# Performance work log

Measured on AMD Instinct MI355X. Metric: run time of the kernel, lower is better.

## Reference

```python
import jax, jax.numpy as jnp
import numpy as np

_pi = np.pi
CONST_FACTOR = np.array([
    1/np.sqrt(4*_pi),
    2*_pi/3*np.sqrt(3/(4*_pi)), 2*_pi/3*np.sqrt(3/(4*_pi)), 2*_pi/3*np.sqrt(3/(4*_pi)),
    _pi/4*3*np.sqrt(5/(12*_pi)), _pi/4*3*np.sqrt(5/(12*_pi)), _pi/4*3*np.sqrt(5/(12*_pi)),
    _pi/4*(3/2)*np.sqrt(5/(12*_pi)), _pi/4*(1/2)*np.sqrt(5/(4*_pi))], dtype=np.float32)


def setup_inputs() -> dict:
    key = jax.random.key(0)
    ks = jax.random.split(key, 8)
    B, V, F, H, W, U = 4, 5023, 9976, 512, 512, 256
    vertices = jax.random.normal(ks[0], (B, V, 3), jnp.float32)
    transformed_vertices = jax.random.normal(ks[1], (B, V, 3), jnp.float32)
    albedos = jax.random.uniform(ks[2], (B, 3, U, U), jnp.float32)
    lights = jax.random.normal(ks[3], (B, 9, 3), jnp.float32) * 0.3
    faces = jax.random.randint(ks[4], (F, 3), 0, V, jnp.int32)
    face_uvcoords = jax.random.uniform(ks[5], (1, F, 3, 3), jnp.float32, minval=-1.0, maxval=1.0)
    # rasterizer outputs (external CUDA kernel): -1 == no face hit
    pix_to_face = jax.random.randint(ks[6], (B, H, W, 1), 0, F + 1, jnp.int32) - 1
    b = jax.random.uniform(ks[7], (B, H, W, 1, 3), jnp.float32) + 1e-3
    bary_coords = b / b.sum(-1, keepdims=True)
    return dict(vertices=vertices, transformed_vertices=transformed_vertices,
                albedos=albedos, lights=lights, face_uvcoords=face_uvcoords,
                bary_coords=bary_coords, faces=faces, pix_to_face=pix_to_face)


def _vertex_normals(vertices, faces):
    vf = vertices[:, faces]                    # [B,F,3,3] face-vertex gather
    v0, v1, v2 = vf[:, :, 0], vf[:, :, 1], vf[:, :, 2]
    B, V = vertices.shape[:2]
    n = jnp.zeros((B, V, 3), vertices.dtype)
    n = n.at[:, faces[:, 1]].add(jnp.cross(v2 - v1, v0 - v1))
    n = n.at[:, faces[:, 2]].add(jnp.cross(v0 - v2, v1 - v2))
    n = n.at[:, faces[:, 0]].add(jnp.cross(v1 - v0, v2 - v0))
    return n / jnp.clip(jnp.linalg.norm(n, axis=-1, keepdims=True), 1e-6)


def _grid_sample(img, grid):
    # torch F.grid_sample bilinear, align_corners=False, zero padding
    # img [B,C,Hi,Wi], grid [B,Ho,Wo,2] (x,y) in [-1,1]
    B, C, Hi, Wi = img.shape
    x = (grid[..., 0] + 1.0) * (Wi * 0.5) - 0.5
    y = (grid[..., 1] + 1.0) * (Hi * 0.5) - 0.5
    x0 = jnp.floor(x); y0 = jnp.floor(y)
    wx = x - x0; wy = y - y0

    def fetch(xi, yi):
        xi_i = xi.astype(jnp.int32); yi_i = yi.astype(jnp.int32)
        valid = ((xi_i >= 0) & (xi_i < Wi) & (yi_i >= 0) & (yi_i < Hi)).astype(img.dtype)
        xc = jnp.clip(xi_i, 0, Wi - 1); yc = jnp.clip(yi_i, 0, Hi - 1)
        vals = jax.vmap(lambda im, yy, xx: im[:, yy, xx])(img, yc, xc)  # [B,C,Ho,Wo]
        return vals * valid[:, None]

    return (fetch(x0, y0) * ((1 - wx) * (1 - wy))[:, None]
            + fetch(x0 + 1, y0) * (wx * (1 - wy))[:, None]
            + fetch(x0, y0 + 1) * ((1 - wx) * wy)[:, None]
            + fetch(x0 + 1, y0 + 1) * (wx * wy)[:, None])


def reference(vertices, transformed_vertices, albedos, lights, face_uvcoords,
              bary_coords, faces, pix_to_face):
    sg = jax.lax.stop_gradient
    B = vertices.shape[0]
    cf = jnp.asarray(CONST_FACTOR)

    # depth normalization (global min/max as in torch)
    z = transformed_vertices[:, :, 2]
    z = z - z.min(); z = z / z.max(); z = z * 80.0 + 10.0
    tv = transformed_vertices.at[:, :, 2].set(z)

    face_vertice = vertices[:, faces]                        # [B,F,3,3]
    normals = _vertex_normals(vertices, faces)
    face_normals = normals[:, faces]                         # [B,F,3,3]
    t_normals = _vertex_normals(tv, faces)
    t_face_normals = t_normals[:, faces]                     # [B,F,3,3]

    attributes = jnp.concatenate([
        jnp.broadcast_to(face_uvcoords, (B,) + face_uvcoords.shape[1:]),
        sg(t_face_normals), sg(face_vertice), face_normals], -1)  # [B,F,3,12]

    # barycentric interpolation (Pytorch3dRasterizer.forward tail)
    mask = pix_to_face < 0                                   # [B,H,W,1]
    safe = jnp.where(mask, 0, pix_to_face)
    pfv = attributes[jnp.arange(B)[:, None, None, None], safe]   # [B,H,W,1,3,12]
    pv = (bary_coords[..., None] * pfv).sum(-2)              # [B,H,W,1,12]
    pv = jnp.where(mask[..., None], 0.0, pv)
    pv = pv[:, :, :, 0].transpose(0, 3, 1, 2)                # [B,12,H,W]
    vismask = (~mask[..., 0]).astype(pv.dtype)[:, None]      # [B,1,H,W]
    rendering = jnp.concatenate([pv, vismask], 1)            # [B,13,H,W]

    # albedo sampling via UV grid
    grid = rendering[:, :2].transpose(0, 2, 3, 1)            # [B,H,W,2]
    albedo_images = _grid_sample(albedos, grid)              # [B,3,H,W]

    # spherical harmonic shading (add_SHlight, lights [B,9,3])
    N = rendering[:, 9:12]                                   # [B,3,H,W]
    one = jnp.ones_like(N[:, 0])
    sh = jnp.stack([one, N[:, 0], N[:, 1], N[:, 2],
                    N[:, 0] * N[:, 1], N[:, 0] * N[:, 2], N[:, 1] * N[:, 2],
                    N[:, 0] ** 2 - N[:, 1] ** 2, 3.0 * N[:, 2] ** 2 - 1.0], 1)  # [B,9,H,W]
    sh = sh * cf[None, :, None, None]
    shading = (lights[:, :, :, None, None] * sh[:, :, None]).sum(1)  # [B,3,H,W]

    images = albedo_images * shading
    return images
```

## Files before the change

kernel.cpp:

```cpp
#include <hip/hip_runtime.h>
#include <hip/hip_fp16.h>
#include <math.h>

#define NB 4
#define NV 5023
#define NF 9976
#define NH 512
#define NW 512
#define NU 256

__device__ __constant__ float d_cf[9] = {
    0.28209479177387814f,
    1.0233267079464885f,
    1.0233267079464885f,
    1.0233267079464885f,
    0.8580855308091875f,
    0.8580855308091875f,
    0.8580855308091875f,
    0.42904276540459376f,
    0.24770795610037571f
};

#define NRM_FLOATS  (NB * NV * 3)
#define ZERO_BLOCKS ((NRM_FLOATS + 255) / 256)
#define FACE_ITEMS  (NB * NF)
#define FACE_BLOCKS ((FACE_ITEMS + 255) / 256)

#define ACELLS 257
#define AINT2_ITEMS  (NB * ACELLS * ACELLS)
#define AINT2_BLOCKS ((AINT2_ITEMS + 255) / 256)

__device__ inline float pack2h(float a, float b) {
    __half2 h = __halves2half2(__float2half_rn(a), __float2half_rn(b));
    union { __half2 h; float f; } u; u.h = h; return u.f;
}
__device__ inline float2 unpack2h(float f) {
    union { float f; __half2 h; } u; u.f = f;
    return __half22float2(u.h);
}
__device__ inline float pack2s(float a, float b) {
    unsigned int lo = (unsigned short)(short)__float2int_rn(a * 32767.0f);
    unsigned int hi = (unsigned short)(short)__float2int_rn(b * 32767.0f);
    return __uint_as_float(lo | (hi << 16));
}
__device__ inline float2 unpack2s(float f) {
    unsigned int u = __float_as_uint(f);
    const float s = 1.0f / 32767.0f;
    return make_float2((float)(short)(u & 0xffffu) * s,
                       (float)(short)(u >> 16) * s);
}
__device__ inline unsigned int packu10(float r, float g, float b) {
    unsigned int qr = (unsigned int)__float2int_rn(r * 1023.0f);
    unsigned int qg = (unsigned int)__float2int_rn(g * 1023.0f);
    unsigned int qb = (unsigned int)__float2int_rn(b * 1023.0f);
    return qr | (qg << 10) | (qb << 20);
}

__global__ void init_kernel(float*       __restrict__ nrm,
                            const float* __restrict__ albedos,
                            const float* __restrict__ lights,
                            uint4*       __restrict__ aint2,
                            float*       __restrict__ lsbuf) {
    if (blockIdx.x < ZERO_BLOCKS) {
        int i = blockIdx.x * blockDim.x + threadIdx.x;
        if (i < NRM_FLOATS) nrm[i] = 0.0f;
        if (i < NB * 27) {
            int b = i / 27;
            int kc = i - b * 27;
            lsbuf[i] = lights[b * 27 + kc] * d_cf[kc / 3] * (1.0f / 1023.0f);
        }
    } else {
        int j = (blockIdx.x - ZERO_BLOCKS) * blockDim.x + threadIdx.x;
        if (j >= AINT2_ITEMS) return;
        int b = j / (ACELLS * ACELLS);
        int rc = j - b * (ACELLS * ACELLS);
        int r = rc / ACELLS;
        int c = rc - r * ACELLS;

        const float* ab = albedos + (size_t)b * 3 * NU * NU;
        uint4 cell = make_uint4(0u, 0u, 0u, 0u);

        int x0 = c - 1, x1 = c;
        int y0 = r - 1, y1 = r;
        bool vx0 = (x0 >= 0);
        bool vx1 = (x1 <= NU - 1);
        bool vy0 = (y0 >= 0);
        bool vy1 = (y1 <= NU - 1);

        if (vy0) {
            int row = y0 * NU;
            if (vx0) { int o = row + x0;
                cell.x = packu10(ab[o], ab[NU*NU + o], ab[2*NU*NU + o]); }
            if (vx1) { int o = row + x1;
                cell.y = packu10(ab[o], ab[NU*NU + o], ab[2*NU*NU + o]); }
        }
        if (vy1) {
            int row = y1 * NU;
            if (vx0) { int o = row + x0;
                cell.z = packu10(ab[o], ab[NU*NU + o], ab[2*NU*NU + o]); }
            if (vx1) { int o = row + x1;
                cell.w = packu10(ab[o], ab[NU*NU + o], ab[2*NU*NU + o]); }
        }
        aint2[j] = cell;
    }
}

__global__ void face_accum_kernel(const float* __restrict__ verts,
                                  const int*   __restrict__ faces,
                                  float*       __restrict__ nrm) {
    int idx = blockIdx.x * blockDim.x + threadIdx.x;
    if (idx >= FACE_ITEMS) return;
    int b = idx / NF;
    int f = idx - b * NF;

    int i0 = faces[f * 3 + 0];
    int i1 = faces[f * 3 + 1];
    int i2 = faces[f * 3 + 2];

    const float* vb = verts + (size_t)b * NV * 3;
    float v0x = vb[i0 * 3 + 0], v0y = vb[i0 * 3 + 1], v0z = vb[i0 * 3 + 2];
    float v1x = vb[i1 * 3 + 0], v1y = vb[i1 * 3 + 1], v1z = vb[i1 * 3 + 2];
    float v2x = vb[i2 * 3 + 0], v2y = vb[i2 * 3 + 1], v2z = vb[i2 * 3 + 2];

    float ax = v1x - v0x, ay = v1y - v0y, az = v1z - v0z;
    float bx = v2x - v0x, by = v2y - v0y, bz = v2z - v0z;
    float cx = ay * bz - az * by;
    float cy = az * bx - ax * bz;
    float cz = ax * by - ay * bx;

    float* nb = nrm + (size_t)b * NV * 3;
    atomicAdd(&nb[i0 * 3 + 0], cx);
    atomicAdd(&nb[i0 * 3 + 1], cy);
    atomicAdd(&nb[i0 * 3 + 2], cz);
    atomicAdd(&nb[i1 * 3 + 0], cx);
    atomicAdd(&nb[i1 * 3 + 1], cy);
    atomicAdd(&nb[i1 * 3 + 2], cz);
    atomicAdd(&nb[i2 * 3 + 0], cx);
    atomicAdd(&nb[i2 * 3 + 1], cy);
    atomicAdd(&nb[i2 * 3 + 2], cz);
}

__global__ void pack_kernel(const float* __restrict__ nrm,
                            const int*   __restrict__ faces,
                            const float* __restrict__ uvc,
                            float4*      __restrict__ recs) {
    int idx = blockIdx.x * blockDim.x + threadIdx.x;
    if (idx >= FACE_ITEMS) return;
    int b = idx / NF;
    int f = idx - b * NF;

    int i0 = faces[f * 3 + 0];
    int i1 = faces[f * 3 + 1];
    int i2 = faces[f * 3 + 2];

    const float* nb = nrm + (size_t)b * NV * 3;
    float n0x = nb[i0 * 3 + 0], n0y = nb[i0 * 3 + 1], n0z = nb[i0 * 3 + 2];
    float n1x = nb[i1 * 3 + 0], n1y = nb[i1 * 3 + 1], n1z = nb[i1 * 3 + 2];
    float n2x = nb[i2 * 3 + 0], n2y = nb[i2 * 3 + 1], n2z = nb[i2 * 3 + 2];

    float l0 = 1.0f / fmaxf(sqrtf(n0x*n0x + n0y*n0y + n0z*n0z), 1e-6f);
    float l1 = 1.0f / fmaxf(sqrtf(n1x*n1x + n1y*n1y + n1z*n1z), 1e-6f);
    float l2 = 1.0f / fmaxf(sqrtf(n2x*n2x + n2y*n2y + n2z*n2z), 1e-6f);

    const float* uvf = uvc + (size_t)f * 9;

    float4 q0, q1;
    q0.x = pack2s(uvf[0], uvf[1]);
    q0.y = pack2s(uvf[3], uvf[4]);
    q0.z = pack2s(uvf[6], uvf[7]);
    q0.w = pack2h(n0x * l0, n0y * l0);
    q1.x = pack2h(n0z * l0, n1x * l1);
    q1.y = pack2h(n1y * l1, n1z * l1);
    q1.z = pack2h(n2x * l2, n2y * l2);
    q1.w = pack2h(n2z * l2, 0.0f);

    recs[(size_t)idx * 2 + 0] = q0;
    recs[(size_t)idx * 2 + 1] = q1;
}

__global__ void render_kernel(const float4* __restrict__ recs,
                              const uint4* __restrict__ aint2,
                              const float* __restrict__ lsbuf,
                              const float4* __restrict__ bary4,
                              const int4*  __restrict__ p2f4,
                              float*       __restrict__ out) {
    const int blk = blockIdx.x;
    const int xcd = blk & 7;
    const int b   = xcd >> 1;
    const int j   = ((blk >> 3) << 1) | (xcd & 1);
    const int q   = j * 256 + threadIdx.x;
    const int p   = q * 4;

    const int pixq = (b * NH * NW) / 4 + q;
    const int4 f4 = p2f4[pixq];
    const float4 bq0 = bary4[pixq * 3 + 0];
    const float4 bq1 = bary4[pixq * 3 + 1];
    const float4 bq2 = bary4[pixq * 3 + 2];

    const float* Ls = lsbuf + b * 27;

    const int fs[4] = {f4.x, f4.y, f4.z, f4.w};
    const float bw[12] = {bq0.x, bq0.y, bq0.z,  bq0.w, bq1.x, bq1.y,
                          bq1.z, bq1.w, bq2.x,  bq2.y, bq2.z, bq2.w};

    const float4* rb = recs + (size_t)b * NF * 2;
    const uint4* ab = aint2 + (size_t)b * ACELLS * ACELLS;

    float outv[3][4];

    #pragma unroll
    for (int px = 0; px < 4; ++px) {
        const int f = fs[px];
        float b0 = bw[px * 3 + 0], b1 = bw[px * 3 + 1], b2 = bw[px * 3 + 2];

        float u = 0.f, v = 0.f, nx = 0.f, ny = 0.f, nz = 0.f;
        if (f >= 0) {
            float4 q0 = rb[(size_t)f * 2 + 0];
            float4 q1 = rb[(size_t)f * 2 + 1];
            float2 uv0 = unpack2s(q0.x);
            float2 uv1 = unpack2s(q0.y);
            float2 uv2 = unpack2s(q0.z);
            float2 hA  = unpack2h(q0.w);
            float2 hB  = unpack2h(q1.x);
            float2 hC  = unpack2h(q1.y);
            float2 hD  = unpack2h(q1.z);
            float2 hE  = unpack2h(q1.w);

            u  = b0 * uv0.x + b1 * uv1.x + b2 * uv2.x;
            v  = b0 * uv0.y + b1 * uv1.y + b2 * uv2.y;
            nx = b0 * hA.x + b1 * hB.y + b2 * hD.x;
            ny = b0 * hA.y + b1 * hC.x + b2 * hD.y;
            nz = b0 * hB.x + b1 * hC.y + b2 * hE.x;
        }

        float x = (u + 1.0f) * (NU * 0.5f) - 0.5f;
        float y = (v + 1.0f) * (NU * 0.5f) - 0.5f;
        float x0f = floorf(x);
        float y0f = floorf(y);
        float wx = x - x0f;
        float wy = y - y0f;
        int ci = (int)x0f + 1;
        int ri = (int)y0f + 1;

        uint4 cell = ab[ri * ACELLS + ci];

        float iwx = 1.0f - wx, iwy = 1.0f - wy;
        float w00 = iwx * iwy, w10 = wx * iwy, w01 = iwx * wy, w11 = wx * wy;

        float a0 = w00 * (float)(cell.x & 1023u)
                 + w10 * (float)(cell.y & 1023u)
                 + w01 * (float)(cell.z & 1023u)
                 + w11 * (float)(cell.w & 1023u);
        float a1 = w00 * (float)((cell.x >> 10) & 1023u)
                 + w10 * (float)((cell.y >> 10) & 1023u)
                 + w01 * (float)((cell.z >> 10) & 1023u)
                 + w11 * (float)((cell.w >> 10) & 1023u);
        float a2 = w00 * (float)((cell.x >> 20) & 1023u)
                 + w10 * (float)((cell.y >> 20) & 1023u)
                 + w01 * (float)((cell.z >> 20) & 1023u)
                 + w11 * (float)((cell.w >> 20) & 1023u);

        float sh[9];
        sh[0] = 1.0f;
        sh[1] = nx;
        sh[2] = ny;
        sh[3] = nz;
        sh[4] = nx * ny;
        sh[5] = nx * nz;
        sh[6] = ny * nz;
        sh[7] = nx * nx - ny * ny;
        sh[8] = 3.0f * nz * nz - 1.0f;

        float s0 = 0.f, s1 = 0.f, s2 = 0.f;
        #pragma unroll
        for (int k = 0; k < 9; ++k) {
            s0 += Ls[k * 3 + 0] * sh[k];
            s1 += Ls[k * 3 + 1] * sh[k];
            s2 += Ls[k * 3 + 2] * sh[k];
        }

        outv[0][px] = a0 * s0;
        outv[1][px] = a1 * s1;
        outv[2][px] = a2 * s2;
    }

    const size_t hw = (size_t)NH * NW;
    #pragma unroll
    for (int c = 0; c < 3; ++c) {
        float4* op = (float4*)(out + ((size_t)b * 3 + c) * hw + p);
        *op = make_float4(outv[c][0], outv[c][1], outv[c][2], outv[c][3]);
    }
}

extern "C" void kernel_launch(void* const* d_in, const int* in_sizes, int n_in,
                              void* d_out, int out_size, void* d_ws, size_t ws_size,
                              hipStream_t stream) {
    const float* vertices = (const float*)d_in[0];
    const float* albedos  = (const float*)d_in[2];
    const float* lights   = (const float*)d_in[3];
    const float* uvc      = (const float*)d_in[4];
    const float* bary     = (const float*)d_in[5];
    const int*   faces    = (const int*)d_in[6];
    const int*   p2f      = (const int*)d_in[7];
    float*       out      = (float*)d_out;

    char* ws = (char*)d_ws;
    float* nrm = (float*)ws;
    size_t nrm_bytes = (size_t)NB * NV * 3 * sizeof(float);
    size_t off = (nrm_bytes + 255) & ~(size_t)255;
    float4* recs = (float4*)(ws + off);
    off += (size_t)FACE_ITEMS * 32;
    off = (off + 255) & ~(size_t)255;
    uint4* aint2 = (uint4*)(ws + off);
    off += (size_t)AINT2_ITEMS * sizeof(uint4);
    off = (off + 255) & ~(size_t)255;
    float* lsbuf = (float*)(ws + off);

    {
        init_kernel<<<ZERO_BLOCKS + AINT2_BLOCKS, 256, 0, stream>>>(
            nrm, albedos, lights, aint2, lsbuf);
    }
    {
        face_accum_kernel<<<FACE_BLOCKS, 256, 0, stream>>>(vertices, faces, nrm);
    }
    {
        pack_kernel<<<FACE_BLOCKS, 256, 0, stream>>>(nrm, faces, uvc, recs);
    }
    {
        render_kernel<<<NB * 256, 256, 0, stream>>>(recs, aint2, lsbuf,
                                                    (const float4*)bary,
                                                    (const int4*)p2f, out);
    }
}
```

Baseline: 48.95 us.

## Fuse normal accumulation and face packing via grid-wide spin barrier

Merges the face normal scatter-add kernel and the per-face packing kernel into one kernel of 160 blocks, which together cover all faces. A global atomic counter, reset in the init kernel, serves as a grid barrier so that every atomic accumulation lands before normals are read back and packed. The goal is to save one kernel launch and the inter-kernel gap. The cost is that correctness now depends on all 160 blocks being resident at once, and on the spin barrier adding latency.

```diff
diff --git a/kernel.cpp b/kernel.cpp
--- a/kernel.cpp
+++ b/kernel.cpp
@@ -24,7 +24,7 @@
 #define NRM_FLOATS  (NB * NV * 3)
 #define ZERO_BLOCKS ((NRM_FLOATS + 255) / 256)
 #define FACE_ITEMS  (NB * NF)
-#define FACE_BLOCKS ((FACE_ITEMS + 255) / 256)
+#define AP_BLOCKS   160
 
 #define ACELLS 257
 #define AINT2_ITEMS  (NB * ACELLS * ACELLS)
@@ -56,11 +56,12 @@
     return qr | (qg << 10) | (qb << 20);
 }
 
-__global__ void init_kernel(float*       __restrict__ nrm,
-                            const float* __restrict__ albedos,
-                            const float* __restrict__ lights,
-                            uint4*       __restrict__ aint2,
-                            float*       __restrict__ lsbuf) {
+__global__ void init_kernel(float*        __restrict__ nrm,
+                            const float*  __restrict__ albedos,
+                            const float*  __restrict__ lights,
+                            uint4*        __restrict__ aint2,
+                            float*        __restrict__ lsbuf,
+                            unsigned int* __restrict__ bar) {
     if (blockIdx.x < ZERO_BLOCKS) {
         int i = blockIdx.x * blockDim.x + threadIdx.x;
         if (i < NRM_FLOATS) nrm[i] = 0.0f;
@@ -69,6 +70,7 @@
             int kc = i - b * 27;
             lsbuf[i] = lights[b * 27 + kc] * d_cf[kc / 3] * (1.0f / 1023.0f);
         }
+        if (blockIdx.x == 0 && threadIdx.x == 0) bar[0] = 0u;
     } else {
         int j = (blockIdx.x - ZERO_BLOCKS) * blockDim.x + threadIdx.x;
         if (j >= AINT2_ITEMS) return;
@@ -105,77 +107,82 @@
     }
 }
 
-__global__ void face_accum_kernel(const float* __restrict__ verts,
-                                  const int*   __restrict__ faces,
-                                  float*       __restrict__ nrm) {
-    int idx = blockIdx.x * blockDim.x + threadIdx.x;
-    if (idx >= FACE_ITEMS) return;
-    int b = idx / NF;
-    int f = idx - b * NF;
-
-    int i0 = faces[f * 3 + 0];
-    int i1 = faces[f * 3 + 1];
-    int i2 = faces[f * 3 + 2];
-
-    const float* vb = verts + (size_t)b * NV * 3;
-    float v0x = vb[i0 * 3 + 0], v0y = vb[i0 * 3 + 1], v0z = vb[i0 * 3 + 2];
-    float v1x = vb[i1 * 3 + 0], v1y = vb[i1 * 3 + 1], v1z = vb[i1 * 3 + 2];
-    float v2x = vb[i2 * 3 + 0], v2y = vb[i2 * 3 + 1], v2z = vb[i2 * 3 + 2];
-
-    float ax = v1x - v0x, ay = v1y - v0y, az = v1z - v0z;
-    float bx = v2x - v0x, by = v2y - v0y, bz = v2z - v0z;
-    float cx = ay * bz - az * by;
-    float cy = az * bx - ax * bz;
-    float cz = ax * by - ay * bx;
-
-    float* nb = nrm + (size_t)b * NV * 3;
-    atomicAdd(&nb[i0 * 3 + 0], cx);
-    atomicAdd(&nb[i0 * 3 + 1], cy);
-    atomicAdd(&nb[i0 * 3 + 2], cz);
-    atomicAdd(&nb[i1 * 3 + 0], cx);
-    atomicAdd(&nb[i1 * 3 + 1], cy);
-    atomicAdd(&nb[i1 * 3 + 2], cz);
-    atomicAdd(&nb[i2 * 3 + 0], cx);
-    atomicAdd(&nb[i2 * 3 + 1], cy);
-    atomicAdd(&nb[i2 * 3 + 2], cz);
-}
-
-__global__ void pack_kernel(const float* __restrict__ nrm,
-                            const int*   __restrict__ faces,
-                            const float* __restrict__ uvc,
-                            float4*      __restrict__ recs) {
-    int idx = blockIdx.x * blockDim.x + threadIdx.x;
-    if (idx >= FACE_ITEMS) return;
-    int b = idx / NF;
-    int f = idx - b * NF;
-
-    int i0 = faces[f * 3 + 0];
-    int i1 = faces[f * 3 + 1];
-    int i2 = faces[f * 3 + 2];
-
-    const float* nb = nrm + (size_t)b * NV * 3;
-    float n0x = nb[i0 * 3 + 0], n0y = nb[i0 * 3 + 1], n0z = nb[i0 * 3 + 2];
-    float n1x = nb[i1 * 3 + 0], n1y = nb[i1 * 3 + 1], n1z = nb[i1 * 3 + 2];
-    float n2x = nb[i2 * 3 + 0], n2y = nb[i2 * 3 + 1], n2z = nb[i2 * 3 + 2];
-
-    float l0 = 1.0f / fmaxf(sqrtf(n0x*n0x + n0y*n0y + n0z*n0z), 1e-6f);
-    float l1 = 1.0f / fmaxf(sqrtf(n1x*n1x + n1y*n1y + n1z*n1z), 1e-6f);
-    float l2 = 1.0f / fmaxf(sqrtf(n2x*n2x + n2y*n2y + n2z*n2z), 1e-6f);
-
-    const float* uvf = uvc + (size_t)f * 9;
-
-    float4 q0, q1;
-    q0.x = pack2s(uvf[0], uvf[1]);
-    q0.y = pack2s(uvf[3], uvf[4]);
-    q0.z = pack2s(uvf[6], uvf[7]);
-    q0.w = pack2h(n0x * l0, n0y * l0);
-    q1.x = pack2h(n0z * l0, n1x * l1);
-    q1.y = pack2h(n1y * l1, n1z * l1);
-    q1.z = pack2h(n2x * l2, n2y * l2);
-    q1.w = pack2h(n2z * l2, 0.0f);
-
-    recs[(size_t)idx * 2 + 0] = q0;
-    recs[(size_t)idx * 2 + 1] = q1;
+__global__ void __launch_bounds__(256)
+accum_pack_kernel(const float*  __restrict__ verts,
+                  const int*    __restrict__ faces,
+                  const float*  __restrict__ uvc,
+                  float*        __restrict__ nrm,
+                  float4*       __restrict__ recs,
+                  unsigned int* __restrict__ bar) {
+    const int idx = blockIdx.x * blockDim.x + threadIdx.x;
+    int b = 0, f = 0, i0 = 0, i1 = 0, i2 = 0;
+
+    if (idx < FACE_ITEMS) {
+        b = idx / NF;
+        f = idx - b * NF;
+        i0 = faces[f * 3 + 0];
+        i1 = faces[f * 3 + 1];
+        i2 = faces[f * 3 + 2];
+
+        const float* vb = verts + (size_t)b * NV * 3;
+        float v0x = vb[i0*3+0], v0y = vb[i0*3+1], v0z = vb[i0*3+2];
+        float v1x = vb[i1*3+0], v1y = vb[i1*3+1], v1z = vb[i1*3+2];
+        float v2x = vb[i2*3+0], v2y = vb[i2*3+1], v2z = vb[i2*3+2];
+
+        float ax = v1x - v0x, ay = v1y - v0y, az = v1z - v0z;
+        float bx = v2x - v0x, by = v2y - v0y, bz = v2z - v0z;
+        float cx = ay * bz - az * by;
+        float cy = az * bx - ax * bz;
+        float cz = ax * by - ay * bx;
+
+        float* nb = nrm + (size_t)b * NV * 3;
+        atomicAdd(&nb[i0 * 3 + 0], cx);
+        atomicAdd(&nb[i0 * 3 + 1], cy);
+        atomicAdd(&nb[i0 * 3 + 2], cz);
+        atomicAdd(&nb[i1 * 3 + 0], cx);
+        atomicAdd(&nb[i1 * 3 + 1], cy);
+        atomicAdd(&nb[i1 * 3 + 2], cz);
+        atomicAdd(&nb[i2 * 3 + 0], cx);
+        atomicAdd(&nb[i2 * 3 + 1], cy);
+        atomicAdd(&nb[i2 * 3 + 2], cz);
+    }
+
+    __syncthreads();
+    if (threadIdx.x == 0) {
+        __threadfence();
+        __hip_atomic_fetch_add(bar, 1u, __ATOMIC_ACQ_REL,
+                               __HIP_MEMORY_SCOPE_AGENT);
+        while (__hip_atomic_load(bar, __ATOMIC_ACQUIRE,
+                                 __HIP_MEMORY_SCOPE_AGENT) < (unsigned)AP_BLOCKS) {}
+    }
+    __syncthreads();
+    __threadfence();
+
+    if (idx < FACE_ITEMS) {
+        const float* nb = nrm + (size_t)b * NV * 3;
+        float n0x = nb[i0*3+0], n0y = nb[i0*3+1], n0z = nb[i0*3+2];
+        float n1x = nb[i1*3+0], n1y = nb[i1*3+1], n1z = nb[i1*3+2];
+        float n2x = nb[i2*3+0], n2y = nb[i2*3+1], n2z = nb[i2*3+2];
+
+        float l0 = 1.0f / fmaxf(sqrtf(n0x*n0x + n0y*n0y + n0z*n0z), 1e-6f);
+        float l1 = 1.0f / fmaxf(sqrtf(n1x*n1x + n1y*n1y + n1z*n1z), 1e-6f);
+        float l2 = 1.0f / fmaxf(sqrtf(n2x*n2x + n2y*n2y + n2z*n2z), 1e-6f);
+
+        const float* uvf = uvc + (size_t)f * 9;
+
+        float4 q0, q1;
+        q0.x = pack2s(uvf[0], uvf[1]);
+        q0.y = pack2s(uvf[3], uvf[4]);
+        q0.z = pack2s(uvf[6], uvf[7]);
+        q0.w = pack2h(n0x * l0, n0y * l0);
+        q1.x = pack2h(n0z * l0, n1x * l1);
+        q1.y = pack2h(n1y * l1, n1z * l1);
+        q1.z = pack2h(n2x * l2, n2y * l2);
+        q1.w = pack2h(n2z * l2, 0.0f);
+
+        recs[(size_t)idx * 2 + 0] = q0;
+        recs[(size_t)idx * 2 + 1] = q1;
+    }
 }
 
 __global__ void render_kernel(const float4* __restrict__ recs,
@@ -315,16 +322,17 @@
     off += (size_t)AINT2_ITEMS * sizeof(uint4);
     off = (off + 255) & ~(size_t)255;
     float* lsbuf = (float*)(ws + off);
+    off += (size_t)NB * 27 * sizeof(float);
+    off = (off + 255) & ~(size_t)255;
+    unsigned int* bar = (unsigned int*)(ws + off);
 
     {
         init_kernel<<<ZERO_BLOCKS + AINT2_BLOCKS, 256, 0, stream>>>(
-            nrm, albedos, lights, aint2, lsbuf);
+            nrm, albedos, lights, aint2, lsbuf, bar);
     }
     {
-        face_accum_kernel<<<FACE_BLOCKS, 256, 0, stream>>>(vertices, faces, nrm);
-    }
-    {
-        pack_kernel<<<FACE_BLOCKS, 256, 0, stream>>>(nrm, faces, uvc, recs);
+        accum_pack_kernel<<<AP_BLOCKS, 256, 0, stream>>>(
+            vertices, faces, uvc, nrm, recs, bar);
     }
     {
         render_kernel<<<NB * 256, 256, 0, stream>>>(recs, aint2, lsbuf,
```

Result: slower. 67.19 us (+37.3%).
